# Performance work log

Hardware: AMD Instinct MI355X
Metric: run time of the kernel (lower is better)

Reference implementation:

```python
import jax, jax.numpy as jnp
import numpy as np

N_EMBD = 1024
N_HEAD = 16
SEQ_LEN = 2048
BATCH = 4
ROPE_THETA = 10000.0


def _rope_tables(T, hd, dtype=jnp.float32):
    freqs = 1.0 / (ROPE_THETA ** (jnp.arange(0, hd, 2, dtype=jnp.float32) / hd))
    t = jnp.arange(T, dtype=jnp.float32)
    ang = jnp.outer(t, freqs)  # [T, hd//2]
    return jnp.cos(ang).astype(dtype), jnp.sin(ang).astype(dtype)


def _apply_rope(x, cos, sin):
    # x: [B,H,T,hd]; cos/sin: [T, hd//2]
    hd = x.shape[-1]
    x1, x2 = x[..., : hd // 2], x[..., hd // 2 :]
    c = cos[None, None, : x.shape[2], :]
    s = sin[None, None, : x.shape[2], :]
    return jnp.concatenate([x1 * c - x2 * s, x2 * c + x1 * s], axis=-1)


def _rms_norm(x):
    eps = jnp.finfo(x.dtype).eps
    return x * jax.lax.rsqrt(jnp.mean(jnp.square(x), axis=-1, keepdims=True) + eps)


def setup_inputs() -> dict:
    key = jax.random.key(0)
    k1, k2, k3, k4 = jax.random.split(key, 4)
    C = N_EMBD
    x = jax.random.normal(k1, (BATCH, SEQ_LEN, C), dtype=jnp.float32)
    w_attn = jax.random.normal(k2, (C, 3 * C), dtype=jnp.float32) * (1.0 / np.sqrt(C))
    w_proj = jax.random.normal(k3, (C, C), dtype=jnp.float32) * (1.0 / np.sqrt(C))
    val_embed = jax.random.normal(k4, (SEQ_LEN, C), dtype=jnp.float32) * 0.02
    return {"x": x, "w_attn": w_attn, "w_proj": w_proj, "val_embed": val_embed}


def reference(x, w_attn, w_proj, val_embed):
    B, T, C = x.shape
    H = N_HEAD
    hd = C // H

    qkv = x @ w_attn  # [B,T,3C]
    q, k, v = jnp.split(qkv, 3, axis=-1)
    v = v + val_embed[:T]

    def to_heads(t):
        return t.reshape(B, T, H, hd).transpose(0, 2, 1, 3)  # [B,H,T,hd]

    q, k, v = to_heads(q), to_heads(k), to_heads(v)

    cos, sin = _rope_tables(T, hd, x.dtype)
    q = _rms_norm(_apply_rope(q, cos, sin))
    k = _rms_norm(_apply_rope(k, cos, sin))

    scale = 1.0 / np.sqrt(hd)
    scores = jnp.einsum("bhqd,bhkd->bhqk", q, k) * scale  # [B,H,T,T]
    causal = jnp.tril(jnp.ones((T, T), dtype=bool))
    scores = jnp.where(causal[None, None], scores, jnp.finfo(scores.dtype).min)
    attn = jax.nn.softmax(scores, axis=-1)
    y = jnp.einsum("bhqk,bhkd->bhqd", attn, v)  # [B,H,T,hd]
    y = y.transpose(0, 2, 1, 3).reshape(B, T, C)
    return y @ w_proj
```

## Files before the change

### kernel.cpp

```cpp
#include <hip/hip_runtime.h>
#include <float.h>
#include <math.h>

#define BB 4
#define TT 2048
#define CC 1024
#define HH 16
#define HD 64
#define C3 3072

typedef __bf16 bf16;
typedef __bf16 bf16x8 __attribute__((ext_vector_type(8)));
typedef __bf16 bf16x4 __attribute__((ext_vector_type(4)));
typedef float f32x4 __attribute__((ext_vector_type(4)));
typedef float f32x16 __attribute__((ext_vector_type(16)));
typedef unsigned int uint32x4 __attribute__((ext_vector_type(4)));

#define QSCALE 0.18033688f

__device__ __forceinline__ void gload16(const void* g, void* l) {
    __builtin_amdgcn_global_load_lds(
        (const __attribute__((address_space(1))) void*)g,
        (__attribute__((address_space(3))) void*)l, 16, 0, 0);
}

__global__ __launch_bounds__(256) void rope_table_k(float* __restrict__ tab) {
    int idx = blockIdx.x * 256 + threadIdx.x;
    if (idx >= TT * 32) return;
    int t = idx >> 5;
    int j = idx & 31;
    float freq = powf(10000.0f, -((float)(2 * j)) / 64.0f);
    float ang = (float)t * freq;
    tab[idx] = cosf(ang);
    tab[TT * 32 + idx] = sinf(ang);
}

__global__ __launch_bounds__(256) void cvt_f2b_k(const float* __restrict__ in,
                                                 bf16* __restrict__ out, int n8) {
    int i = blockIdx.x * 256 + threadIdx.x;
    if (i >= n8) return;
    const float4* p = (const float4*)(in + (size_t)i * 8);
    float4 a = p[0], b = p[1];
    bf16x8 o;
    o[0] = (bf16)a.x; o[1] = (bf16)a.y; o[2] = (bf16)a.z; o[3] = (bf16)a.w;
    o[4] = (bf16)b.x; o[5] = (bf16)b.y; o[6] = (bf16)b.z; o[7] = (bf16)b.w;
    *(bf16x8*)(out + (size_t)i * 8) = o;
}

__global__ __launch_bounds__(256) void transW_k(const float* __restrict__ in,
                                                bf16* __restrict__ out, int K, int N) {
    __shared__ bf16 tile[64][72];
    int n0 = blockIdx.x * 64, k0 = blockIdx.y * 64;
    int t = threadIdx.x;
    int r = t >> 2, c4 = (t & 3) * 16;
    const float4* src = (const float4*)(in + (size_t)(k0 + r) * N + n0 + c4);
    #pragma unroll
    for (int j = 0; j < 4; ++j) {
        float4 v = src[j];
        tile[r][c4 + 4 * j + 0] = (bf16)v.x; tile[r][c4 + 4 * j + 1] = (bf16)v.y;
        tile[r][c4 + 4 * j + 2] = (bf16)v.z; tile[r][c4 + 4 * j + 3] = (bf16)v.w;
    }
    __syncthreads();
    bf16x8 o0, o1;
    #pragma unroll
    for (int j = 0; j < 8; ++j) o0[j] = tile[c4 + j][r];
    #pragma unroll
    for (int j = 0; j < 8; ++j) o1[j] = tile[c4 + 8 + j][r];
    *(bf16x8*)(out + (size_t)(n0 + r) * K + k0 + c4) = o0;
    *(bf16x8*)(out + (size_t)(n0 + r) * K + k0 + c4 + 8) = o1;
}

__global__ __launch_bounds__(256) void gemm_bt_k(const bf16* __restrict__ A,
                                                 const bf16* __restrict__ BT,
                                                 float* __restrict__ C,
                                                 bf16* __restrict__ Qh,
                                                 bf16* __restrict__ Kh,
                                                 bf16* __restrict__ Vh,
                                                 int M, int N, int K, int epi) {
    __shared__ bf16 Al[128 * 64];
    __shared__ bf16 Bl[128 * 64];
    const int tid = threadIdx.x;
    const int w = tid >> 6, lane = tid & 63;
    const int m0 = blockIdx.y * 128, n0 = blockIdx.x * 128;
    const int wrow = (w >> 1) * 64, wcol = (w & 1) * 64;
    const int srow = lane >> 3;
    const int selem = (((lane & 7) ^ srow) << 3);
    const int xorL = (lane & 7) << 3;

    const f32x4 fz = {0.f, 0.f, 0.f, 0.f};
    f32x4 acc[4][4];
    #pragma unroll
    for (int i = 0; i < 4; ++i)
        #pragma unroll
        for (int j = 0; j < 4; ++j) acc[i][j] = fz;

    for (int k0 = 0; k0 < K; k0 += 64) {
        __syncthreads();
        #pragma unroll
        for (int jj = 0; jj < 4; ++jj) {
            int c = w * 4 + jj;
            int row = c * 8 + srow;
            gload16(A + (size_t)(m0 + row) * K + k0 + selem, &Al[c * 512]);
            gload16(BT + (size_t)(n0 + row) * K + k0 + selem, &Bl[c * 512]);
        }
        __syncthreads();
        #pragma unroll
        for (int kh = 0; kh < 2; ++kh) {
            const int off = (kh * 32 + (lane >> 4) * 8) ^ xorL;
            bf16x8 aF[4], bF[4];
            #pragma unroll
            for (int i = 0; i < 4; ++i) {
                aF[i] = *(const bf16x8*)&Al[(wrow + i * 16 + (lane & 15)) * 64 + off];
                bF[i] = *(const bf16x8*)&Bl[(wcol + i * 16 + (lane & 15)) * 64 + off];
            }
            #pragma unroll
            for (int i = 0; i < 4; ++i)
                #pragma unroll
                for (int j = 0; j < 4; ++j)
                    acc[i][j] = __builtin_amdgcn_mfma_f32_16x16x32_bf16(
                        aF[i], bF[j], acc[i][j], 0, 0, 0);
        }
    }

    if (epi == 0) {
        #pragma unroll
        for (int i = 0; i < 4; ++i)
            #pragma unroll
            for (int r = 0; r < 4; ++r) {
                size_t rowm = (size_t)(m0 + wrow + i * 16 + 4 * (lane >> 4) + r);
                #pragma unroll
                for (int j = 0; j < 4; ++j)
                    C[rowm * N + n0 + wcol + j * 16 + (lane & 15)] = acc[i][j][r];
            }
    } else {
        int ncb = n0 + wcol;
        int region = ncb >> 10;
        int h = (ncb & 1023) >> 6;
        bf16* dst = (region == 0) ? Qh : ((region == 1) ? Kh : Vh);
        #pragma unroll
        for (int i = 0; i < 4; ++i)
            #pragma unroll
            for (int r = 0; r < 4; ++r) {
                int m = m0 + wrow + i * 16 + 4 * (lane >> 4) + r;
                int b = m >> 11, t = m & (TT - 1);
                size_t rb = ((size_t)(b * HH + h) * TT + t) * HD;
                #pragma unroll
                for (int j = 0; j < 4; ++j)
                    dst[rb + j * 16 + (lane & 15)] = (bf16)acc[i][j][r];
            }
    }
}

__global__ __launch_bounds__(256) void rope_rms_k(bf16* __restrict__ Qh,
                                                  bf16* __restrict__ Kh,
                                                  const bf16* __restrict__ Vh,
                                                  bf16* __restrict__ Vt,
                                                  const float* __restrict__ emb,
                                                  const float* __restrict__ tab) {
    __shared__ bf16 tile[64][72];
    const int t0 = blockIdx.x * 64;
    const int bh = blockIdx.y;
    const int h = bh & (HH - 1);
    const int w = threadIdx.x >> 6, lane = threadIdx.x & 63;
    const int j = lane & 31;
    #pragma unroll 4
    for (int i = 0; i < 16; ++i) {
        const int tl = w * 16 + i;
        const int t = t0 + tl;
        const size_t base = ((size_t)bh * TT + t) * HD + lane;
        const float cs = tab[t * 32 + j];
        const float sn = tab[TT * 32 + t * 32 + j];
        float q = (float)Qh[base], k = (float)Kh[base], v = (float)Vh[base];
        float qp = __shfl_xor(q, 32, 64), kp = __shfl_xor(k, 32, 64);
        float rq = (lane < 32) ? q * cs - qp * sn : q * cs + qp * sn;
        float rk = (lane < 32) ? k * cs - kp * sn : k * cs + kp * sn;
        float sq = rq * rq, sk = rk * rk;
        #pragma unroll
        for (int off = 1; off < 64; off <<= 1) {
            sq += __shfl_xor(sq, off, 64);
            sk += __shfl_xor(sk, off, 64);
        }
        rq *= rsqrtf(sq * (1.0f / 64.0f) + 1.1920929e-07f);
        rk *= rsqrtf(sk * (1.0f / 64.0f) + 1.1920929e-07f);
        Qh[base] = (bf16)(rq * QSCALE);
        Kh[base] = (bf16)rk;
        tile[tl][lane] = (bf16)(v + emb[(size_t)t * CC + h * HD + lane]);
    }
    __syncthreads();
    const int tt = threadIdx.x;
    const int r = tt >> 2, c4 = (tt & 3) * 16;
    bf16x8 o0, o1;
    #pragma unroll
    for (int jj = 0; jj < 8; ++jj) o0[jj] = tile[c4 + jj][r];
    #pragma unroll
    for (int jj = 0; jj < 8; ++jj) o1[jj] = tile[c4 + 8 + jj][r];
    bf16* out = Vt + (size_t)bh * HD * TT;
    *(bf16x8*)(out + (size_t)r * TT + t0 + c4) = o0;
    *(bf16x8*)(out + (size_t)r * TT + t0 + c4 + 8) = o1;
}

__global__ __launch_bounds__(512) void attn_k(const bf16* __restrict__ Qh,
                                              const bf16* __restrict__ Kh,
                                              const bf16* __restrict__ Vt,
                                              bf16* __restrict__ Y) {
    const int flat = (int)blockIdx.y * 8 + (int)blockIdx.x;
    const int slot = flat >> 3;
    const int bh = (flat & 7) * 8 + (slot & 7);
    const int qb = 7 - (slot >> 3);
    const int b = bh >> 4, h = bh & 15;
    const int tid = threadIdx.x, w = tid >> 6, lane = tid & 63;
    const int hi = lane >> 5, q31 = lane & 31;
    const int wq0 = qb * 256 + w * 32;
    const int qg = wq0 + q31;
    const int xr = q31 & 7;

    __shared__ bf16 Kl[3][64 * 64];
    __shared__ bf16 Vl[3][64 * 64];

    const bf16* Kbase = Kh + (size_t)bh * TT * HD;
    const bf16* Vbase = Vt + (size_t)bh * HD * TT;

    bf16x8 qF[4];
    {
        const bf16* qp = Qh + (size_t)bh * TT * HD + (size_t)qg * HD + hi * 8;
        #pragma unroll
        for (int ds = 0; ds < 4; ++ds) qF[ds] = *(const bf16x8*)(qp + ds * 16);
    }

    f32x16 accY[2];
    #pragma unroll
    for (int i = 0; i < 16; ++i) { accY[0][i] = 0.f; accY[1][i] = 0.f; }
    float mR = -INFINITY, lR = 0.f;

    const int srow = lane >> 3;
    const int schunk = (lane & 7) ^ srow;
    const int ktN = 4 * qb + 4;

    {
        int r0 = w * 8 + srow;
        gload16(Kbase + (size_t)r0 * HD + schunk * 8, &Kl[0][w * 512]);
        gload16(Vbase + (size_t)r0 * TT + schunk * 8, &Vl[0][w * 512]);
        gload16(Kbase + (size_t)(64 + r0) * HD + schunk * 8, &Kl[1][w * 512]);
        gload16(Vbase + (size_t)r0 * TT + 64 + schunk * 8, &Vl[1][w * 512]);
    }
    asm volatile("s_waitcnt vmcnt(2)" ::: "memory");
    __builtin_amdgcn_s_barrier();
    __builtin_amdgcn_sched_barrier(0);

    int bufC = 0, bufS = 2;
    for (int kt = 0; kt < ktN; ++kt) {
        if (kt + 2 < ktN) {
            int trow = (kt + 2) * 64 + w * 8 + srow;
            int drow = w * 8 + srow;
            gload16(Kbase + (size_t)trow * HD + schunk * 8, &Kl[bufS][w * 512]);
            gload16(Vbase + (size_t)drow * TT + (kt + 2) * 64 + schunk * 8,
                    &Vl[bufS][w * 512]);
        }
        if (kt * 64 <= wq0 + 31) {
            const bf16* KL = &Kl[bufC][0];
            const bf16* VL = &Vl[bufC][0];
            f32x16 sa[2];
            #pragma unroll
            for (int i = 0; i < 16; ++i) { sa[0][i] = 0.f; sa[1][i] = 0.f; }
            __builtin_amdgcn_s_setprio(1);
            #pragma unroll
            for (int ds = 0; ds < 4; ++ds) {
                int cc = ds * 2 + hi;
                bf16x8 k0 = *(const bf16x8*)&KL[q31 * 64 + ((cc ^ xr) * 8)];
                bf16x8 k1 = *(const bf16x8*)&KL[(32 + q31) * 64 + ((cc ^ xr) * 8)];
                sa[0] = __builtin_amdgcn_mfma_f32_32x32x16_bf16(k0, qF[ds], sa[0], 0, 0, 0);
                sa[1] = __builtin_amdgcn_mfma_f32_32x32x16_bf16(k1, qF[ds], sa[1], 0, 0, 0);
            }
            __builtin_amdgcn_s_setprio(0);
            if (kt * 64 + 63 > wq0) {
                #pragma unroll
                for (int kb = 0; kb < 2; ++kb)
                    #pragma unroll
                    for (int r = 0; r < 16; ++r) {
                        int k = kt * 64 + kb * 32 + (r & 3) + 8 * (r >> 2) + 4 * hi;
                        if (k > qg) sa[kb][r] = -1e30f;
                    }
            }
            float mx = -1e30f;
            #pragma unroll
            for (int r = 0; r < 16; ++r) {
                mx = fmaxf(mx, sa[0][r]);
                mx = fmaxf(mx, sa[1][r]);
            }
            mx = fmaxf(mx, __shfl_xor(mx, 32, 64));
            if (!__all(mx - mR <= 12.0f)) {
                float mnew = fmaxf(mR, mx);
                float alpha = __builtin_amdgcn_exp2f(mR - mnew);
                #pragma unroll
                for (int i = 0; i < 16; ++i) { accY[0][i] *= alpha; accY[1][i] *= alpha; }
                lR *= alpha;
                mR = mnew;
            }
            float sum = 0.f;
            #pragma unroll
            for (int kb = 0; kb < 2; ++kb)
                #pragma unroll
                for (int r = 0; r < 16; ++r) {
                    float p = __builtin_amdgcn_exp2f(sa[kb][r] - mR);
                    sa[kb][r] = p;
                    sum += p;
                }
            sum += __shfl_xor(sum, 32, 64);
            lR += sum;
            unsigned int wds[2][8];
            #pragma unroll
            for (int kb = 0; kb < 2; ++kb)
                #pragma unroll
                for (int jj = 0; jj < 8; ++jj) {
                    bf16x8 tmp;
                    tmp[0] = (bf16)sa[kb][2 * jj];
                    tmp[1] = (bf16)sa[kb][2 * jj + 1];
                    wds[kb][jj] = *(unsigned int*)&tmp;
                }
            bf16x8 pF[4];
            #pragma unroll
            for (int ks = 0; ks < 4; ++ks) {
                const int kb = ks >> 1, s = ks & 1;
                unsigned int w0 = wds[kb][4 * s + 0], w1 = wds[kb][4 * s + 1];
                unsigned int w2 = wds[kb][4 * s + 2], w3 = wds[kb][4 * s + 3];
                unsigned int t0 = hi ? w0 : w2, t1 = hi ? w1 : w3;
                unsigned int r0 = (unsigned int)__shfl_xor((int)t0, 32, 64);
                unsigned int r1 = (unsigned int)__shfl_xor((int)t1, 32, 64);
                uint32x4 fw;
                fw[0] = hi ? r0 : w0; fw[1] = hi ? r1 : w1;
                fw[2] = hi ? w2 : r0; fw[3] = hi ? w3 : r1;
                pF[ks] = *(bf16x8*)&fw;
            }
            __builtin_amdgcn_s_setprio(1);
            #pragma unroll
            for (int cd = 0; cd < 2; ++cd) {
                const int rowD = cd * 32 + q31;
                #pragma unroll
                for (int ks = 0; ks < 4; ++ks) {
                    int cc = ks * 2 + hi;
                    bf16x8 vA = *(const bf16x8*)&VL[rowD * 64 + ((cc ^ xr) * 8)];
                    accY[cd] = __builtin_amdgcn_mfma_f32_32x32x16_bf16(
                        vA, pF[ks], accY[cd], 0, 0, 0);
                }
            }
            __builtin_amdgcn_s_setprio(0);
        }
        if (kt + 1 < ktN) {
            if (kt + 2 < ktN) {
                asm volatile("s_waitcnt vmcnt(2)" ::: "memory");
            } else {
                asm volatile("s_waitcnt vmcnt(0)" ::: "memory");
            }
            __builtin_amdgcn_s_barrier();
            __builtin_amdgcn_sched_barrier(0);
        }
        bufC = (bufC == 2) ? 0 : bufC + 1;
        bufS = (bufS == 2) ? 0 : bufS + 1;
    }

    float inv = 1.0f / lR;
    bf16* yp = Y + ((size_t)(b * TT + qg)) * CC + h * HD;
    #pragma unroll
    for (int cd = 0; cd < 2; ++cd)
        #pragma unroll
        for (int g = 0; g < 4; ++g) {
            int d0 = cd * 32 + 8 * g + 4 * hi;
            bf16x4 o;
            o[0] = (bf16)(accY[cd][4 * g + 0] * inv);
            o[1] = (bf16)(accY[cd][4 * g + 1] * inv);
            o[2] = (bf16)(accY[cd][4 * g + 2] * inv);
            o[3] = (bf16)(accY[cd][4 * g + 3] * inv);
            *(bf16x4*)(yp + d0) = o;
        }
}

extern "C" void kernel_launch(void* const* d_in, const int* in_sizes, int n_in,
                              void* d_out, int out_size, void* d_ws, size_t ws_size,
                              hipStream_t stream) {
    const float* x         = (const float*)d_in[0];
    const float* w_attn    = (const float*)d_in[1];
    const float* w_proj    = (const float*)d_in[2];
    const float* val_embed = (const float*)d_in[3];
    float* out = (float*)d_out;

    bf16* xb  = (bf16*)d_ws;
    bf16* waT = xb + (size_t)8192 * 1024;
    bf16* wpT = waT + (size_t)3072 * 1024;
    bf16* Qh  = wpT + (size_t)1024 * 1024;
    bf16* Kh  = Qh + (size_t)64 * 2048 * 64;
    bf16* Vh  = Kh + (size_t)64 * 2048 * 64;
    bf16* Vt  = Vh + (size_t)64 * 2048 * 64;
    bf16* Yb  = Vt + (size_t)64 * 2048 * 64;
    float* tab = (float*)(Yb + (size_t)64 * 2048 * 64);

    rope_table_k<<<dim3((TT * 32 + 255) / 256), dim3(256), 0, stream>>>(tab);
    cvt_f2b_k<<<dim3(8192 * 1024 / 8 / 256), dim3(256), 0, stream>>>(x, xb, 8192 * 1024 / 8);
    transW_k<<<dim3(3072 / 64, 1024 / 64), dim3(256), 0, stream>>>(w_attn, waT, 1024, 3072);
    transW_k<<<dim3(1024 / 64, 1024 / 64), dim3(256), 0, stream>>>(w_proj, wpT, 1024, 1024);
    gemm_bt_k<<<dim3(3072 / 128, 8192 / 128), dim3(256), 0, stream>>>(
        xb, waT, nullptr, Qh, Kh, Vh, 8192, 3072, 1024, 1);
    rope_rms_k<<<dim3(TT / 64, BB * HH), dim3(256), 0, stream>>>(
        Qh, Kh, Vh, Vt, val_embed, tab);
    attn_k<<<dim3(8, BB * HH), dim3(512), 0, stream>>>(Qh, Kh, Vt, Yb);
    gemm_bt_k<<<dim3(1024 / 128, 8192 / 128), dim3(256), 0, stream>>>(
        Yb, wpT, out, nullptr, nullptr, nullptr, 8192, 1024, 1024, 0);
}
```

Measured before the change: 199.3 us.

## Use 256x256 double-buffered GEMM with XCD-aware block remap for QKV projection

Adds a dedicated QKV projection kernel that uses 256x256 output tiles with 512 threads and double-buffered async global-to-LDS loads (128 KB dynamic shared memory). Block indices are remapped so that consecutive tiles land on the same XCD, and MFMA sections are wrapped in priority hints. The aim is more data reuse per tile and overlap of loads with compute. The cost is lower occupancy, one block per CU, on a grid of only 384 blocks. The old GEMM keeps only the fp32 output path for the final projection.

```diff
diff --git a/kernel.cpp b/kernel.cpp
--- a/kernel.cpp
+++ b/kernel.cpp
@@ -70,13 +70,107 @@
     *(bf16x8*)(out + (size_t)(n0 + r) * K + k0 + c4 + 8) = o1;
 }
 
+__global__ __launch_bounds__(512) void gemm256_k(const bf16* __restrict__ A,
+                                                 const bf16* __restrict__ BT,
+                                                 bf16* __restrict__ Qh,
+                                                 bf16* __restrict__ Kh,
+                                                 bf16* __restrict__ Vh,
+                                                 int M, int N, int K) {
+    extern __shared__ bf16 smem[];
+    const int tid = threadIdx.x;
+    const int w = tid >> 6, lane = tid & 63;
+    const int wm = w >> 2, wn = w & 3;
+    const int nwg = (int)gridDim.x;
+    const int cpx = nwg >> 3;
+    const int flat = (int)blockIdx.x;
+    const int wg = (flat & 7) * cpx + (flat >> 3);
+    const int gx = N >> 8;
+    const int n0 = (wg % gx) * 256;
+    const int m0 = (wg / gx) * 256;
+
+    const int srow = lane >> 3;
+    const int schunk = (lane & 7) ^ srow;
+    const int xorL = (lane & 7) << 3;
+    const int KT = K >> 6;
+
+    f32x4 acc[8][4];
+    #pragma unroll
+    for (int i = 0; i < 8; ++i)
+        #pragma unroll
+        for (int j = 0; j < 4; ++j) acc[i][j] = {0.f, 0.f, 0.f, 0.f};
+
+    {
+        bf16* Al = smem;
+        bf16* Bl = smem + 16384;
+        #pragma unroll
+        for (int i = 0; i < 4; ++i) {
+            int row = i * 64 + w * 8;
+            gload16(A + (size_t)(m0 + row + srow) * K + schunk * 8, Al + row * 64);
+            gload16(BT + (size_t)(n0 + row + srow) * K + schunk * 8, Bl + row * 64);
+        }
+    }
+    __syncthreads();
+
+    for (int kt = 0; kt < KT; ++kt) {
+        const int buf = kt & 1;
+        if (kt + 1 < KT) {
+            bf16* Al = smem + (buf ^ 1) * 32768;
+            bf16* Bl = Al + 16384;
+            const int k0 = (kt + 1) * 64;
+            #pragma unroll
+            for (int i = 0; i < 4; ++i) {
+                int row = i * 64 + w * 8;
+                gload16(A + (size_t)(m0 + row + srow) * K + k0 + schunk * 8,
+                        Al + row * 64);
+                gload16(BT + (size_t)(n0 + row + srow) * K + k0 + schunk * 8,
+                        Bl + row * 64);
+            }
+        }
+        const bf16* Al = smem + buf * 32768;
+        const bf16* Bl = Al + 16384;
+        #pragma unroll
+        for (int kh = 0; kh < 2; ++kh) {
+            const int off = (kh * 32 + (lane >> 4) * 8) ^ xorL;
+            bf16x8 aF[8], bF[4];
+            #pragma unroll
+            for (int i = 0; i < 8; ++i)
+                aF[i] = *(const bf16x8*)&Al[(wm * 128 + i * 16 + (lane & 15)) * 64 + off];
+            #pragma unroll
+            for (int j = 0; j < 4; ++j)
+                bF[j] = *(const bf16x8*)&Bl[(wn * 64 + j * 16 + (lane & 15)) * 64 + off];
+            __builtin_amdgcn_s_setprio(1);
+            #pragma unroll
+            for (int i = 0; i < 8; ++i)
+                #pragma unroll
+                for (int j = 0; j < 4; ++j)
+                    acc[i][j] = __builtin_amdgcn_mfma_f32_16x16x32_bf16(
+                        aF[i], bF[j], acc[i][j], 0, 0, 0);
+            __builtin_amdgcn_s_setprio(0);
+        }
+        __syncthreads();
+    }
+
+    const int ncb = n0 + wn * 64;
+    const int region = ncb >> 10;
+    const int h = (ncb & 1023) >> 6;
+    bf16* dst = (region == 0) ? Qh : ((region == 1) ? Kh : Vh);
+    #pragma unroll
+    for (int i = 0; i < 8; ++i)
+        #pragma unroll
+        for (int r = 0; r < 4; ++r) {
+            int m = m0 + wm * 128 + i * 16 + 4 * (lane >> 4) + r;
+            int b = m >> 11, t = m & (TT - 1);
+            size_t rb = ((size_t)(b * HH + h) * TT + t) * HD;
+            #pragma unroll
+            for (int j = 0; j < 4; ++j)
+                dst[rb + j * 16 + (lane & 15)] = (bf16)acc[i][j][r];
+        }
+}
+
 __global__ __launch_bounds__(256) void gemm_bt_k(const bf16* __restrict__ A,
                                                  const bf16* __restrict__ BT,
                                                  float* __restrict__ C,
-                                                 bf16* __restrict__ Qh,
-                                                 bf16* __restrict__ Kh,
-                                                 bf16* __restrict__ Vh,
-                                                 int M, int N, int K, int epi) {
+                                                 int M, int N, int K) {
     __shared__ bf16 Al[128 * 64];
     __shared__ bf16 Bl[128 * 64];
     const int tid = threadIdx.x;
@@ -122,33 +216,15 @@
         }
     }
 
-    if (epi == 0) {
-        #pragma unroll
-        for (int i = 0; i < 4; ++i)
-            #pragma unroll
-            for (int r = 0; r < 4; ++r) {
-                size_t rowm = (size_t)(m0 + wrow + i * 16 + 4 * (lane >> 4) + r);
-                #pragma unroll
-                for (int j = 0; j < 4; ++j)
-                    C[rowm * N + n0 + wcol + j * 16 + (lane & 15)] = acc[i][j][r];
-            }
-    } else {
-        int ncb = n0 + wcol;
-        int region = ncb >> 10;
-        int h = (ncb & 1023) >> 6;
-        bf16* dst = (region == 0) ? Qh : ((region == 1) ? Kh : Vh);
-        #pragma unroll
-        for (int i = 0; i < 4; ++i)
-            #pragma unroll
-            for (int r = 0; r < 4; ++r) {
-                int m = m0 + wrow + i * 16 + 4 * (lane >> 4) + r;
-                int b = m >> 11, t = m & (TT - 1);
-                size_t rb = ((size_t)(b * HH + h) * TT + t) * HD;
-                #pragma unroll
-                for (int j = 0; j < 4; ++j)
-                    dst[rb + j * 16 + (lane & 15)] = (bf16)acc[i][j][r];
-            }
-    }
+    #pragma unroll
+    for (int i = 0; i < 4; ++i)
+        #pragma unroll
+        for (int r = 0; r < 4; ++r) {
+            size_t rowm = (size_t)(m0 + wrow + i * 16 + 4 * (lane >> 4) + r);
+            #pragma unroll
+            for (int j = 0; j < 4; ++j)
+                C[rowm * N + n0 + wcol + j * 16 + (lane & 15)] = acc[i][j][r];
+        }
 }
 
 __global__ __launch_bounds__(256) void rope_rms_k(bf16* __restrict__ Qh,
@@ -393,15 +469,18 @@
     bf16* Yb  = Vt + (size_t)64 * 2048 * 64;
     float* tab = (float*)(Yb + (size_t)64 * 2048 * 64);
 
+    hipFuncSetAttribute((const void*)gemm256_k,
+                        hipFuncAttributeMaxDynamicSharedMemorySize, 131072);
+
     rope_table_k<<<dim3((TT * 32 + 255) / 256), dim3(256), 0, stream>>>(tab);
     cvt_f2b_k<<<dim3(8192 * 1024 / 8 / 256), dim3(256), 0, stream>>>(x, xb, 8192 * 1024 / 8);
     transW_k<<<dim3(3072 / 64, 1024 / 64), dim3(256), 0, stream>>>(w_attn, waT, 1024, 3072);
     transW_k<<<dim3(1024 / 64, 1024 / 64), dim3(256), 0, stream>>>(w_proj, wpT, 1024, 1024);
-    gemm_bt_k<<<dim3(3072 / 128, 8192 / 128), dim3(256), 0, stream>>>(
-        xb, waT, nullptr, Qh, Kh, Vh, 8192, 3072, 1024, 1);
+    gemm256_k<<<dim3((8192 / 256) * (3072 / 256)), dim3(512), 131072, stream>>>(
+        xb, waT, Qh, Kh, Vh, 8192, 3072, 1024);
     rope_rms_k<<<dim3(TT / 64, BB * HH), dim3(256), 0, stream>>>(
         Qh, Kh, Vh, Vt, val_embed, tab);
     attn_k<<<dim3(8, BB * HH), dim3(512), 0, stream>>>(Qh, Kh, Vt, Yb);
     gemm_bt_k<<<dim3(1024 / 128, 8192 / 128), dim3(256), 0, stream>>>(
-        Yb, wpT, out, nullptr, nullptr, nullptr, 8192, 1024, 1024, 0);
-}
+        Yb, wpT, out, 8192, 1024, 1024);
+}
```

Measured after the change: 194.6 us. 1.02x faster.
